# Optimization experiments

Hardware: AMD Instinct MI355X
Metric: run time of the kernel (lower is better)

Reference implementation:

```python
import jax, jax.numpy as jnp
import numpy as np

D_MODEL = 1024
NUM_HEADS = 16
HEAD_DIM = D_MODEL // NUM_HEADS
MAX_SEQ_LEN = 2048
THETA = 10000.0
BATCH = 2
SEQ = 2048


def _rope_tables():
    inv_freq = 1.0 / (THETA ** (jnp.arange(0, HEAD_DIM, 2, dtype=jnp.float32) / HEAD_DIM))
    pos = jnp.arange(MAX_SEQ_LEN, dtype=jnp.float32)
    freqs = pos[:, None] * inv_freq[None, :]  # [max_seq, head_dim/2]
    return jnp.sin(freqs), jnp.cos(freqs)


def _apply_rope(x, sin, cos):
    # x: [b, h, s, d]; sin/cos: [s, d/2] -> broadcast over b, h
    sin = sin[None, None, :, :]
    cos = cos[None, None, :, :]
    x_even = x[..., 0::2]
    x_odd = x[..., 1::2]
    out_even = x_even * cos - x_odd * sin
    out_odd = x_even * sin + x_odd * cos
    # interleave back: stack on new last axis then flatten
    out = jnp.stack((out_even, out_odd), axis=-1)
    return out.reshape(x.shape)


def setup_inputs() -> dict:
    key = jax.random.key(0)
    ks = jax.random.split(key, 5)
    std = (2.0 / (D_MODEL + D_MODEL)) ** 0.5
    return {
        "x": jax.random.normal(ks[0], (BATCH, SEQ, D_MODEL), dtype=jnp.float32),
        "Wq": jax.random.normal(ks[1], (D_MODEL, D_MODEL), dtype=jnp.float32) * std,
        "Wk": jax.random.normal(ks[2], (D_MODEL, D_MODEL), dtype=jnp.float32) * std,
        "Wv": jax.random.normal(ks[3], (D_MODEL, D_MODEL), dtype=jnp.float32) * std,
        "Wo": jax.random.normal(ks[4], (D_MODEL, D_MODEL), dtype=jnp.float32) * std,
    }


def reference(x, Wq, Wk, Wv, Wo):
    b, s, _ = x.shape
    # projections: weight stored [out, in] as in the torch Linear
    Q = jnp.einsum('bsd,od->bso', x, Wq)
    K = jnp.einsum('bsd,od->bso', x, Wk)
    V = jnp.einsum('bsd,od->bso', x, Wv)
    # split heads -> [b, h, s, hd]
    def split(t):
        return t.reshape(b, s, NUM_HEADS, HEAD_DIM).transpose(0, 2, 1, 3)
    Q, K, V = split(Q), split(K), split(V)
    sin, cos = _rope_tables()
    sin, cos = sin[:s], cos[:s]
    Q = _apply_rope(Q, sin, cos)
    K = _apply_rope(K, sin, cos)
    scale = 1.0 / jnp.sqrt(jnp.float32(HEAD_DIM))
    scores = jnp.einsum('bhqd,bhkd->bhqk', Q, K)
    causal = jnp.tril(jnp.ones((s, s), dtype=bool))[None, None]
    scores = jnp.where(causal, scores, -jnp.inf) * scale  # -inf * scale stays -inf
    attn = jax.nn.softmax(scores, axis=-1)
    out = jnp.einsum('bhqk,bhkd->bhqd', attn, V)
    out = out.transpose(0, 2, 1, 3).reshape(b, s, D_MODEL)
    return jnp.einsum('bsd,od->bso', out, Wo)
```

## Files before the change

### kernel.cpp

```cpp
#include <hip/hip_runtime.h>
#include <math.h>

#define NHEADS 16
#define HD 64
#define SEQ 2048
#define BATCH 2
#define DM 1024
#define MTOT (BATCH*SEQ)
#define LDP 72

typedef __bf16 bf16x8 __attribute__((ext_vector_type(8)));
typedef __bf16 bf16x4 __attribute__((ext_vector_type(4)));
typedef float  f32x4  __attribute__((ext_vector_type(4)));

#define LOG2E 1.4426950408889634f

#define GLD16(gp, lp) __builtin_amdgcn_global_load_lds( \
    (const __attribute__((address_space(1))) void*)(gp), \
    (__attribute__((address_space(3))) void*)(lp), 16, 0, 0)

__global__ __launch_bounds__(256)
void cast_all(const float* __restrict__ x, const float* __restrict__ Wq,
              const float* __restrict__ Wk, const float* __restrict__ Wv,
              const float* __restrict__ Wo,
              __bf16* __restrict__ xb, __bf16* __restrict__ Wqkvb,
              __bf16* __restrict__ Wob)
{
    const size_t NX = (size_t)MTOT * DM;
    const size_t NW = (size_t)DM * DM;
    const size_t i = ((size_t)blockIdx.x * 256 + threadIdx.x) * 8;
    const float* src; __bf16* dst; size_t off;
    if (i < NX)               { src = x;  dst = xb;           off = i; }
    else if (i < NX + NW)     { src = Wq; dst = Wqkvb;        off = i - NX; }
    else if (i < NX + 2*NW)   { src = Wk; dst = Wqkvb + NW;   off = i - NX - NW; }
    else if (i < NX + 3*NW)   { src = Wv; dst = Wqkvb + 2*NW; off = i - NX - 2*NW; }
    else                      { src = Wo; dst = Wob;          off = i - NX - 3*NW; }
    const float4 f0 = *(const float4*)&src[off];
    const float4 f1 = *(const float4*)&src[off + 4];
    bf16x8 o;
    o[0] = (__bf16)f0.x; o[1] = (__bf16)f0.y; o[2] = (__bf16)f0.z; o[3] = (__bf16)f0.w;
    o[4] = (__bf16)f1.x; o[5] = (__bf16)f1.y; o[6] = (__bf16)f1.z; o[7] = (__bf16)f1.w;
    *(bf16x8*)&dst[off] = o;
}

template<int BM, int BN, int MODE>
__global__ __launch_bounds__(256, 4)
void gemm_mfma(const __bf16* __restrict__ A, const __bf16* __restrict__ W,
               float* __restrict__ Cf,
               __bf16* __restrict__ Qb, __bf16* __restrict__ Kb,
               __bf16* __restrict__ Vtb)
{
    constexpr int IT = BM / 32;
    constexpr int JT = BN / 32;
    __shared__ __bf16 As[BM * 64];
    __shared__ __bf16 Bs[BN * 64];

    const int tid  = threadIdx.x;
    const int lane = tid & 63;
    const int wave = tid >> 6;
    const int ll   = lane & 15;
    const int quad = lane >> 4;
    const int wm   = (wave & 1) * (BM / 2);
    const int wn   = (wave >> 1) * (BN / 2);
    const int bm   = blockIdx.x * BM;
    const int bn   = blockIdx.y * BN;

    const __bf16* Ab = A + (size_t)bm * DM;
    const __bf16* Wb = W + (size_t)bn * DM;

    f32x4 acc[IT][JT];
#pragma unroll
    for (int i = 0; i < IT; i++)
#pragma unroll
        for (int j = 0; j < JT; j++) acc[i][j] = (f32x4){0.f, 0.f, 0.f, 0.f};

    for (int k0 = 0; k0 < DM; k0 += 64) {
#pragma unroll
        for (int j = 0; j < BM / 32; j++) {
            const int t = tid + 256 * j;
            const int r = t >> 3, g = t & 7;
            GLD16(Ab + (size_t)r * DM + k0 + ((g ^ (r & 7)) * 8), &As[t * 8]);
        }
#pragma unroll
        for (int j = 0; j < BN / 32; j++) {
            const int t = tid + 256 * j;
            const int r = t >> 3, g = t & 7;
            GLD16(Wb + (size_t)r * DM + k0 + ((g ^ (r & 7)) * 8), &Bs[t * 8]);
        }
        __syncthreads();

#pragma unroll
        for (int kh = 0; kh < 2; kh++) {
            bf16x8 af[IT], bfr[JT];
#pragma unroll
            for (int i = 0; i < IT; i++) {
                const int r = wm + i*16 + ll;
                const int g = kh*4 + quad;
                af[i] = *(const bf16x8*)&As[(r*8 + (g ^ (r & 7))) * 8];
            }
#pragma unroll
            for (int j = 0; j < JT; j++) {
                const int r = wn + j*16 + ll;
                const int g = kh*4 + quad;
                bfr[j] = *(const bf16x8*)&Bs[(r*8 + (g ^ (r & 7))) * 8];
            }
#pragma unroll
            for (int i = 0; i < IT; i++)
#pragma unroll
                for (int j = 0; j < JT; j++)
                    acc[i][j] = __builtin_amdgcn_mfma_f32_16x16x32_bf16(
                        af[i], bfr[j], acc[i][j], 0, 0, 0);
        }
        __syncthreads();
    }

    if (MODE == 1) {
#pragma unroll
        for (int i = 0; i < IT; i++) {
#pragma unroll
            for (int j = 0; j < JT; j++) {
                const int gc = bn + wn + j*16 + ll;
#pragma unroll
                for (int r = 0; r < 4; r++) {
                    const int gr = bm + wm + i*16 + quad*4 + r;
                    Cf[(size_t)gr * DM + gc] = acc[i][j][r];
                }
            }
        }
    } else {
        const int which = bn >> 10;
        const int nb = bn & 1023;
#pragma unroll
        for (int i = 0; i < IT; i++) {
            const int m0 = bm + wm + i*16 + quad*4;
            const int b  = m0 >> 11;
            const int s0 = m0 & (SEQ - 1);
#pragma unroll
            for (int j = 0; j < JT; j++) {
                const int n_g = nb + wn + j*16 + ll;
                const int h = n_g >> 6, d = n_g & (HD - 1);
                if (which == 2) {
                    bf16x4 pk;
#pragma unroll
                    for (int r = 0; r < 4; r++) pk[r] = (__bf16)acc[i][j][r];
                    *(bf16x4*)&Vtb[((size_t)((b*NHEADS + h)*HD + d)) * SEQ + s0] = pk;
                } else {
                    __bf16* P = (which == 0) ? Qb : Kb;
                    const float sc = (which == 0) ? 0.125f * LOG2E : 1.0f;
                    const float inv =
                        exp2f(-(float)(d & ~1) * (13.287712379549449f / 64.0f));
                    const bool odd = (d & 1);
#pragma unroll
                    for (int r = 0; r < 4; r++) {
                        const float own = acc[i][j][r];
                        const float oth = __shfl_xor(own, 1);
                        float sn, cs;
                        __sincosf((float)(s0 + r) * inv, &sn, &cs);
                        const float xe = odd ? oth : own;
                        const float xo = odd ? own : oth;
                        const float o = odd ? (xe * sn + xo * cs)
                                            : (xe * cs - xo * sn);
                        P[((size_t)(b*NHEADS + h) * SEQ + s0 + r) * HD + d] =
                            (__bf16)(o * sc);
                    }
                }
            }
        }
    }
}

__global__ __launch_bounds__(256, 2)
void attn_mfma(const __bf16* __restrict__ Qb, const __bf16* __restrict__ Kb,
               const __bf16* __restrict__ Vtb, __bf16* __restrict__ AOb)
{
    __shared__ __align__(16) __bf16 pt[4][2][16][LDP];
    __shared__ float comb[4][64][17];
    __shared__ float lbuf[4][64];

    const int tid  = threadIdx.x;
    const int wave = tid >> 6;
    const int lane = tid & 63;
    const int m    = lane & 15;
    const int quad = lane >> 4;
    const int bh   = blockIdx.x;
    const int b    = bh >> 4, h = bh & 15;
    const int qb   = blockIdx.z ? (SEQ/64 - 1) - (int)blockIdx.y : (int)blockIdx.y;
    const int q0   = qb * 64;

    const __bf16* Qp = Qb + (size_t)bh * SEQ * HD;
    const __bf16* Kp = Kb + (size_t)bh * SEQ * HD;
    const __bf16* Vp = Vtb + (size_t)bh * HD * SEQ;

    bf16x8 ones;
#pragma unroll
    for (int j = 0; j < 8; j++) ones[j] = (__bf16)1.0f;

    bf16x8 qf[4][2];
#pragma unroll
    for (int i = 0; i < 4; i++) {
        const __bf16* qp = Qp + (size_t)(q0 + i*16 + m) * HD + quad*8;
        qf[i][0] = *(const bf16x8*)qp;
        qf[i][1] = *(const bf16x8*)(qp + 32);
    }

    f32x4 acc[4][4];
    f32x4 l_acc[4];
#pragma unroll
    for (int i = 0; i < 4; i++) {
        l_acc[i] = (f32x4){0.f, 0.f, 0.f, 0.f};
#pragma unroll
        for (int nt = 0; nt < 4; nt++) acc[i][nt] = (f32x4){0.f, 0.f, 0.f, 0.f};
    }

    for (int t = wave; t <= qb; t += 4) {
        const int k0 = t * 64;
        const bool diag = (t == qb);

        bf16x8 kf[4][2], vf[4][2];
#pragma unroll
        for (int tk = 0; tk < 4; tk++) {
            const __bf16* kp = Kp + (size_t)(k0 + tk*16 + m) * HD + quad*8;
            kf[tk][0] = *(const bf16x8*)kp;
            kf[tk][1] = *(const bf16x8*)(kp + 32);
            const __bf16* vp = Vp + (size_t)(tk*16 + m) * SEQ + k0 + quad*8;
            vf[tk][0] = *(const bf16x8*)vp;
            vf[tk][1] = *(const bf16x8*)(vp + 32);
        }

#pragma unroll
        for (int i = 0; i < 4; i++) {
            const int pb = i & 1;
            f32x4 s[4];
#pragma unroll
            for (int tk = 0; tk < 4; tk++) {
                s[tk] = (f32x4){0.f, 0.f, 0.f, 0.f};
                s[tk] = __builtin_amdgcn_mfma_f32_16x16x32_bf16(
                    qf[i][0], kf[tk][0], s[tk], 0, 0, 0);
                s[tk] = __builtin_amdgcn_mfma_f32_16x16x32_bf16(
                    qf[i][1], kf[tk][1], s[tk], 0, 0, 0);
            }
#pragma unroll
            for (int tk = 0; tk < 4; tk++) {
#pragma unroll
                for (int r = 0; r < 4; r++) {
                    float sv = s[tk][r];
                    if (diag)
                        sv = (16*tk + m <= 16*i + quad*4 + r) ? sv : -INFINITY;
                    const float p = __builtin_amdgcn_exp2f(sv);
                    pt[wave][pb][quad*4 + r][16*tk + m] = (__bf16)p;
                }
            }
            const bf16x8 af0 = *(const bf16x8*)&pt[wave][pb][m][quad*8];
            const bf16x8 af1 = *(const bf16x8*)&pt[wave][pb][m][32 + quad*8];
            l_acc[i] = __builtin_amdgcn_mfma_f32_16x16x32_bf16(
                af0, ones, l_acc[i], 0, 0, 0);
            l_acc[i] = __builtin_amdgcn_mfma_f32_16x16x32_bf16(
                af1, ones, l_acc[i], 0, 0, 0);
#pragma unroll
            for (int nt = 0; nt < 4; nt++) {
                acc[i][nt] = __builtin_amdgcn_mfma_f32_16x16x32_bf16(
                    af0, vf[nt][0], acc[i][nt], 0, 0, 0);
                acc[i][nt] = __builtin_amdgcn_mfma_f32_16x16x32_bf16(
                    af1, vf[nt][1], acc[i][nt], 0, 0, 0);
            }
        }
    }

    if (m == 0) {
#pragma unroll
        for (int i = 0; i < 4; i++)
#pragma unroll
            for (int r = 0; r < 4; r++)
                lbuf[wave][i*16 + quad*4 + r] = l_acc[i][r];
    }
    __syncthreads();

    const int row = tid >> 2;
    const int c0  = (tid & 3) * 4;
    const float rl = 1.0f / (lbuf[0][row] + lbuf[1][row]
                           + lbuf[2][row] + lbuf[3][row]);
    __bf16* op = AOb + (size_t)(b * SEQ + q0 + row) * DM + h * HD;

#pragma unroll
    for (int nt = 0; nt < 4; nt++) {
#pragma unroll
        for (int i = 0; i < 4; i++)
#pragma unroll
            for (int r = 0; r < 4; r++)
                comb[wave][i*16 + quad*4 + r][m] = acc[i][nt][r];
        __syncthreads();
        bf16x4 ov;
#pragma unroll
        for (int cc = 0; cc < 4; cc++) {
            const int col = c0 + cc;
            const float o = comb[0][row][col] + comb[1][row][col]
                          + comb[2][row][col] + comb[3][row][col];
            ov[cc] = (__bf16)(o * rl);
        }
        *(bf16x4*)&op[nt*16 + c0] = ov;
        if (nt < 3) __syncthreads();
    }
}

extern "C" void kernel_launch(void* const* d_in, const int* in_sizes, int n_in,
                              void* d_out, int out_size, void* d_ws, size_t ws_size,
                              hipStream_t stream) {
    const float* x  = (const float*)d_in[0];
    const float* Wq = (const float*)d_in[1];
    const float* Wk = (const float*)d_in[2];
    const float* Wv = (const float*)d_in[3];
    const float* Wo = (const float*)d_in[4];
    float* out = (float*)d_out;

    char* ws = (char*)d_ws;
    __bf16* xb    = (__bf16*)ws;
    __bf16* Wqkvb = (__bf16*)(ws + ((size_t)8  << 20));
    __bf16* Wob   = (__bf16*)(ws + ((size_t)14 << 20));
    __bf16* Qb    = (__bf16*)(ws + ((size_t)16 << 20));
    __bf16* Kb    = (__bf16*)(ws + ((size_t)24 << 20));
    __bf16* Vtb   = (__bf16*)(ws + ((size_t)32 << 20));
    __bf16* AOb   = (__bf16*)(ws + ((size_t)40 << 20));

    cast_all<<<4096, 256, 0, stream>>>(x, Wq, Wk, Wv, Wo, xb, Wqkvb, Wob);

    gemm_mfma<64,128,0><<<dim3(MTOT/64, 3072/128), 256, 0, stream>>>(
        xb, Wqkvb, nullptr, Qb, Kb, Vtb);

    attn_mfma<<<dim3(BATCH*NHEADS, SEQ/128, 2), 256, 0, stream>>>(
        Qb, Kb, Vtb, AOb);

    gemm_mfma<64,64,1><<<dim3(MTOT/64, DM/64), 256, 0, stream>>>(
        AOb, Wob, out, nullptr, nullptr, nullptr);
}
```

Baseline: 174.6 us.

## Shrink attention query tile to 32 rows and process keys in half-tiles

The attention kernel now handles 32 query rows per block instead of 64, doubling the grid, and splits each 64-key tile into two 32-key halves so fewer K/V fragments are live at once. Launch bounds go from 2 to 3 blocks per CU so the lower register use can raise occupancy and balance the causal workload better. The cost is that each K/V tile is loaded by twice as many blocks, and the output writes become scalar bf16 stores instead of 4-wide vectors. Half of the diagonal tile is masked work for 32-row blocks.

New measurement: 199.3 us. 14.1% more time.

```diff
diff --git a/kernel.cpp b/kernel.cpp
--- a/kernel.cpp
+++ b/kernel.cpp
@@ -169,13 +169,13 @@
     }
 }
 
-__global__ __launch_bounds__(256, 2)
+__global__ __launch_bounds__(256, 3)
 void attn_mfma(const __bf16* __restrict__ Qb, const __bf16* __restrict__ Kb,
                const __bf16* __restrict__ Vtb, __bf16* __restrict__ AOb)
 {
     __shared__ __align__(16) __bf16 pt[4][2][16][LDP];
-    __shared__ float comb[4][64][17];
-    __shared__ float lbuf[4][64];
+    __shared__ float comb[4][32][17];
+    __shared__ float lbuf[4][32];
 
     const int tid  = threadIdx.x;
     const int wave = tid >> 6;
@@ -184,8 +184,8 @@
     const int quad = lane >> 4;
     const int bh   = blockIdx.x;
     const int b    = bh >> 4, h = bh & 15;
-    const int qb   = blockIdx.z ? (SEQ/64 - 1) - (int)blockIdx.y : (int)blockIdx.y;
-    const int q0   = qb * 64;
+    const int qb   = blockIdx.z ? (SEQ/32 - 1) - (int)blockIdx.y : (int)blockIdx.y;
+    const int q0   = qb * 32;
 
     const __bf16* Qp = Qb + (size_t)bh * SEQ * HD;
     const __bf16* Kp = Kb + (size_t)bh * SEQ * HD;
@@ -195,88 +195,91 @@
 #pragma unroll
     for (int j = 0; j < 8; j++) ones[j] = (__bf16)1.0f;
 
-    bf16x8 qf[4][2];
-#pragma unroll
-    for (int i = 0; i < 4; i++) {
+    bf16x8 qf[2][2];
+#pragma unroll
+    for (int i = 0; i < 2; i++) {
         const __bf16* qp = Qp + (size_t)(q0 + i*16 + m) * HD + quad*8;
         qf[i][0] = *(const bf16x8*)qp;
         qf[i][1] = *(const bf16x8*)(qp + 32);
     }
 
-    f32x4 acc[4][4];
-    f32x4 l_acc[4];
-#pragma unroll
-    for (int i = 0; i < 4; i++) {
+    f32x4 acc[2][4];
+    f32x4 l_acc[2];
+#pragma unroll
+    for (int i = 0; i < 2; i++) {
         l_acc[i] = (f32x4){0.f, 0.f, 0.f, 0.f};
 #pragma unroll
         for (int nt = 0; nt < 4; nt++) acc[i][nt] = (f32x4){0.f, 0.f, 0.f, 0.f};
     }
 
-    for (int t = wave; t <= qb; t += 4) {
+    const int tmax = qb >> 1;
+    for (int t = wave; t <= tmax; t += 4) {
         const int k0 = t * 64;
-        const bool diag = (t == qb);
-
-        bf16x8 kf[4][2], vf[4][2];
-#pragma unroll
-        for (int tk = 0; tk < 4; tk++) {
-            const __bf16* kp = Kp + (size_t)(k0 + tk*16 + m) * HD + quad*8;
-            kf[tk][0] = *(const bf16x8*)kp;
-            kf[tk][1] = *(const bf16x8*)(kp + 32);
-            const __bf16* vp = Vp + (size_t)(tk*16 + m) * SEQ + k0 + quad*8;
-            vf[tk][0] = *(const bf16x8*)vp;
-            vf[tk][1] = *(const bf16x8*)(vp + 32);
-        }
-
-#pragma unroll
-        for (int i = 0; i < 4; i++) {
-            const int pb = i & 1;
-            f32x4 s[4];
-#pragma unroll
-            for (int tk = 0; tk < 4; tk++) {
-                s[tk] = (f32x4){0.f, 0.f, 0.f, 0.f};
-                s[tk] = __builtin_amdgcn_mfma_f32_16x16x32_bf16(
-                    qf[i][0], kf[tk][0], s[tk], 0, 0, 0);
-                s[tk] = __builtin_amdgcn_mfma_f32_16x16x32_bf16(
-                    qf[i][1], kf[tk][1], s[tk], 0, 0, 0);
-            }
-#pragma unroll
-            for (int tk = 0; tk < 4; tk++) {
-#pragma unroll
-                for (int r = 0; r < 4; r++) {
-                    float sv = s[tk][r];
-                    if (diag)
-                        sv = (16*tk + m <= 16*i + quad*4 + r) ? sv : -INFINITY;
-                    const float p = __builtin_amdgcn_exp2f(sv);
-                    pt[wave][pb][quad*4 + r][16*tk + m] = (__bf16)p;
+        const bool diag = (t == tmax);
+
+#pragma unroll
+        for (int hh = 0; hh < 2; hh++) {
+            bf16x8 kf2[2][2], vf2[4];
+#pragma unroll
+            for (int tk2 = 0; tk2 < 2; tk2++) {
+                const __bf16* kp =
+                    Kp + (size_t)(k0 + (2*hh + tk2)*16 + m) * HD + quad*8;
+                kf2[tk2][0] = *(const bf16x8*)kp;
+                kf2[tk2][1] = *(const bf16x8*)(kp + 32);
+            }
+#pragma unroll
+            for (int nt = 0; nt < 4; nt++) {
+                const __bf16* vp =
+                    Vp + (size_t)(nt*16 + m) * SEQ + k0 + 32*hh + quad*8;
+                vf2[nt] = *(const bf16x8*)vp;
+            }
+
+#pragma unroll
+            for (int i = 0; i < 2; i++) {
+                f32x4 s2[2];
+#pragma unroll
+                for (int tk2 = 0; tk2 < 2; tk2++) {
+                    s2[tk2] = (f32x4){0.f, 0.f, 0.f, 0.f};
+                    s2[tk2] = __builtin_amdgcn_mfma_f32_16x16x32_bf16(
+                        qf[i][0], kf2[tk2][0], s2[tk2], 0, 0, 0);
+                    s2[tk2] = __builtin_amdgcn_mfma_f32_16x16x32_bf16(
+                        qf[i][1], kf2[tk2][1], s2[tk2], 0, 0, 0);
                 }
-            }
-            const bf16x8 af0 = *(const bf16x8*)&pt[wave][pb][m][quad*8];
-            const bf16x8 af1 = *(const bf16x8*)&pt[wave][pb][m][32 + quad*8];
-            l_acc[i] = __builtin_amdgcn_mfma_f32_16x16x32_bf16(
-                af0, ones, l_acc[i], 0, 0, 0);
-            l_acc[i] = __builtin_amdgcn_mfma_f32_16x16x32_bf16(
-                af1, ones, l_acc[i], 0, 0, 0);
-#pragma unroll
-            for (int nt = 0; nt < 4; nt++) {
-                acc[i][nt] = __builtin_amdgcn_mfma_f32_16x16x32_bf16(
-                    af0, vf[nt][0], acc[i][nt], 0, 0, 0);
-                acc[i][nt] = __builtin_amdgcn_mfma_f32_16x16x32_bf16(
-                    af1, vf[nt][1], acc[i][nt], 0, 0, 0);
+#pragma unroll
+                for (int tk2 = 0; tk2 < 2; tk2++) {
+                    const int kk = k0 + (2*hh + tk2)*16 + m;
+#pragma unroll
+                    for (int r = 0; r < 4; r++) {
+                        float sv = s2[tk2][r];
+                        if (diag)
+                            sv = (kk <= q0 + 16*i + quad*4 + r) ? sv : -INFINITY;
+                        const float p = __builtin_amdgcn_exp2f(sv);
+                        pt[wave][i][quad*4 + r][(2*hh + tk2)*16 + m] = (__bf16)p;
+                    }
+                }
+                const bf16x8 af =
+                    *(const bf16x8*)&pt[wave][i][m][32*hh + quad*8];
+                l_acc[i] = __builtin_amdgcn_mfma_f32_16x16x32_bf16(
+                    af, ones, l_acc[i], 0, 0, 0);
+#pragma unroll
+                for (int nt = 0; nt < 4; nt++)
+                    acc[i][nt] = __builtin_amdgcn_mfma_f32_16x16x32_bf16(
+                        af, vf2[nt], acc[i][nt], 0, 0, 0);
             }
         }
     }
 
     if (m == 0) {
 #pragma unroll
-        for (int i = 0; i < 4; i++)
+        for (int i = 0; i < 2; i++)
 #pragma unroll
             for (int r = 0; r < 4; r++)
                 lbuf[wave][i*16 + quad*4 + r] = l_acc[i][r];
     }
     __syncthreads();
 
-    const int row = tid >> 2;
-    const int c0  = (tid & 3) * 4;
+    const int row = tid >> 3;
+    const int c0  = (tid & 7) * 2;
     const float rl = 1.0f / (lbuf[0][row] + lbuf[1][row]
                            + lbuf[2][row] + lbuf[3][row]);
     __bf16* op = AOb + (size_t)(b * SEQ + q0 + row) * DM + h * HD;
@@ -284,20 +287,18 @@
 #pragma unroll
     for (int nt = 0; nt < 4; nt++) {
 #pragma unroll
-        for (int i = 0; i < 4; i++)
+        for (int i = 0; i < 2; i++)
 #pragma unroll
             for (int r = 0; r < 4; r++)
                 comb[wave][i*16 + quad*4 + r][m] = acc[i][nt][r];
         __syncthreads();
-        bf16x4 ov;
-#pragma unroll
-        for (int cc = 0; cc < 4; cc++) {
+#pragma unroll
+        for (int cc = 0; cc < 2; cc++) {
             const int col = c0 + cc;
             const float o = comb[0][row][col] + comb[1][row][col]
                           + comb[2][row][col] + comb[3][row][col];
-            ov[cc] = (__bf16)(o * rl);
-        }
-        *(bf16x4*)&op[nt*16 + c0] = ov;
+            op[nt*16 + col] = (__bf16)(o * rl);
+        }
         if (nt < 3) __syncthreads();
     }
 }
@@ -326,7 +327,7 @@
     gemm_mfma<64,128,0><<<dim3(MTOT/64, 3072/128), 256, 0, stream>>>(
         xb, Wqkvb, nullptr, Qb, Kb, Vtb);
 
-    attn_mfma<<<dim3(BATCH*NHEADS, SEQ/128, 2), 256, 0, stream>>>(
+    attn_mfma<<<dim3(BATCH*NHEADS, SEQ/64, 2), 256, 0, stream>>>(
         Qb, Kb, Vtb, AOb);
 
     gemm_mfma<64,64,1><<<dim3(MTOT/64, DM/64), 256, 0, stream>>>(
```
